# Optimization experiments

Hardware: AMD Instinct MI355X
Metric: run time of the kernel (lower is better)

## Reference

```python
import jax, jax.numpy as jnp
import numpy as np

N, E, FE = 20000, 160000, 500000
IN, HC, HEADS = 128, 64, 4
HEADC = HC // HEADS          # 16
DV = HEADC                   # 16
KHOP = 3
NUM_T = 128
OUT = 1
CST = 1e-5


def _lin(key, fan_in, fan_out):
    kw, kb = jax.random.split(key)
    s = 1.0 / np.sqrt(fan_in)
    W = jax.random.uniform(kw, (fan_in, fan_out), minval=-s, maxval=s, dtype=jnp.float32)
    b = jax.random.uniform(kb, (fan_out,), minval=-s, maxval=s, dtype=jnp.float32)
    return W, b


def setup_inputs() -> dict:
    key = jax.random.key(0)
    ks = jax.random.split(key, 16)
    x = jax.random.normal(ks[0], (N, IN), dtype=jnp.float32)
    edge_index = jax.random.randint(ks[1], (2, E), 0, N, dtype=jnp.int32)
    full_edge_index = jax.random.randint(ks[2], (2, FE), 0, N, dtype=jnp.int32)
    time_steps = jax.random.randint(ks[3], (N,), 0, NUM_T, dtype=jnp.int32)
    Wi, bi = _lin(ks[4], IN, HC)
    Wt1, bt1 = _lin(ks[5], HC, 4 * HC)
    Wt2, bt2 = _lin(ks[6], 4 * HC, HC)
    WQ, bQ = _lin(ks[7], HC, HEADS * HEADC)
    WK, bK = _lin(ks[8], HC, HEADS * HEADC)
    WV, bV = _lin(ks[9], HC, HEADS * DV)
    Wo, bo = _lin(ks[10], HEADS * DV, DV)
    hopwise = jnp.ones((KHOP + 1,), dtype=jnp.float32)
    headwise = jnp.zeros((HEADS, KHOP), dtype=jnp.float32)
    Wf1, bf1 = _lin(ks[11], 2 * DV, DV)
    Wf2, bf2 = _lin(ks[12], DV, OUT)
    return dict(x=x, edge_index=edge_index, full_edge_index=full_edge_index,
                time_steps=time_steps, Wi=Wi, bi=bi, Wt1=Wt1, bt1=bt1,
                Wt2=Wt2, bt2=bt2, WQ=WQ, bQ=bQ, WK=WK, bK=bK, WV=WV, bV=bV,
                Wo=Wo, bo=bo, hopwise=hopwise, headwise=headwise,
                Wf1=Wf1, bf1=bf1, Wf2=Wf2, bf2=bf2)


def _sin_emb(t, dim, num_steps, rescale=4000.0):
    # Sinusoidal timestep embedding rescaled by num_steps (diffusion style).
    t = t.astype(jnp.float32) * (rescale / num_steps)
    half = dim // 2
    freqs = jnp.exp(-jnp.log(10000.0) / (half - 1) * jnp.arange(half, dtype=jnp.float32))
    args = t[:, None] * freqs[None, :]
    return jnp.concatenate([jnp.sin(args), jnp.cos(args)], axis=-1)


def reference(x, edge_index, full_edge_index, time_steps,
              Wi, bi, Wt1, bt1, Wt2, bt2, WQ, bQ, WK, bK, WV, bV,
              Wo, bo, hopwise, headwise, Wf1, bf1, Wf2, bf2):
    n = x.shape[0]
    row, col = edge_index[0], edge_index[1]

    # random-walk norm: deg over destination (col), norm gathered at source (row)
    deg = jax.ops.segment_sum(jnp.ones_like(col, dtype=x.dtype), col, num_segments=n)
    deg_inv = jnp.where(deg > 0, 1.0 / deg, 0.0)
    norm = deg_inv[row]                                   # [E]

    t_emb = _sin_emb(time_steps, HC, NUM_T)               # [N, HC]
    t_emb = jax.nn.silu(t_emb @ Wt1 + bt1) @ Wt2 + bt2    # [N, HC]

    h = jax.nn.relu(x @ Wi + bi + t_emb)                  # [N, HC]

    Q = (1.0 + jax.nn.elu(h @ WQ + bQ)).reshape(n, HEADS, HEADC)
    Kf = (1.0 + jax.nn.elu(h @ WK + bK)).reshape(n, HEADS, HEADC)
    V = (h @ WV + bV).reshape(n, HEADS, DV)

    M = jnp.einsum('nhi,nhj->nhij', Kf, V)                # [N, H, hc, dv]
    hidden = V * hopwise[0]
    layerwise = jax.nn.softmax(headwise, axis=0)          # softmax over heads

    for hop in range(KHOP):
        # gather-scale-scatter message passing (random walk propagation)
        M = jax.ops.segment_sum(M[row] * norm[:, None, None, None], col, num_segments=n)
        Kf = jax.ops.segment_sum(Kf[row] * norm[:, None, None], col, num_segments=n)
        H = jnp.einsum('nhi,nhij->nhj', Q, M)             # [N, H, dv]
        C = jnp.einsum('nhi,nhi->nh', Q, Kf)[..., None] + CST
        gamma = hopwise[hop + 1] * layerwise[:, hop][:, None]   # [H, 1]
        hidden = hidden + gamma * (H / C)

    # multi_concat output projection
    hidden = hidden.reshape(n, HEADS * DV) @ Wo + bo      # [N, DV]

    src, dst = full_edge_index[0], full_edge_index[1]
    he = jnp.concatenate([hidden[src], hidden[dst]], axis=-1)  # [FE, 2*DV]
    edge_logits = jax.nn.silu(he @ Wf1 + bf1) @ Wf2 + bf2      # [FE, OUT]
    return edge_logits, hidden
```

## Files before the change

### kernel.cpp

```cpp
#include <hip/hip_runtime.h>
#include <hip/hip_bf16.h>
#include <math.h>


#define HC 64
#define HEADS 4
#define HEADC 16
#define DV 16
#define KHOP 3
#define NUM_T 128
#define MSZ 1024
#define SLOTS 64
#define CST 1e-5f

typedef float f32x2 __attribute__((ext_vector_type(2)));

__device__ __forceinline__ float bf2f(unsigned short s) { return __uint_as_float(((unsigned int)s) << 16); }
__device__ __forceinline__ unsigned short f2bf(float f) {
    unsigned int u = __float_as_uint(f);
    u = (u + 0x7fffu + ((u >> 16) & 1u)) >> 16;
    return (unsigned short)u;
}
__device__ __forceinline__ unsigned int pack4fp8(float a, float b, float c, float d) {
    int r = __builtin_amdgcn_cvt_pk_fp8_f32(a, b, 0, false);
    r = __builtin_amdgcn_cvt_pk_fp8_f32(c, d, r, true);
    return (unsigned int)r;
}

__global__ void k_fill(const int* __restrict__ row, const int* __restrict__ col,
                       int* __restrict__ cnt, int* __restrict__ csr, int E) {
    int e = blockIdx.x * 256 + threadIdx.x;
    if (e >= E) return;
    int c = col[e];
    int r = row[e];
    int k = atomicAdd(&cnt[c], 1);
    if (k < SLOTS) csr[c * SLOTS + k] = r;
}

__global__ __launch_bounds__(256) void k_misc(
    const float* __restrict__ Wt1, const float* __restrict__ bt1,
    const float* __restrict__ Wt2, const float* __restrict__ bt2,
    const float* __restrict__ hopwise, const float* __restrict__ headwise,
    const int* __restrict__ cnt,
    float* __restrict__ gamma, float* __restrict__ table,
    float* __restrict__ inv_deg, int n) {
    if (blockIdx.x >= 32) {
        int i = (blockIdx.x - 32) * 256 + threadIdx.x;
        if (i < n) {
            int d = cnt[i];
            inv_deg[i] = (d > 0) ? 1.0f / (float)min(d, SLOTS) : 0.0f;
        }
        return;
    }
    if (blockIdx.x == 0 && threadIdx.x == 0) {
        for (int k = 0; k < KHOP; k++) {
            float m = -1e30f;
            for (int h2 = 0; h2 < HEADS; h2++) m = fmaxf(m, headwise[h2 * KHOP + k]);
            float ex[HEADS]; float s = 0.f;
            for (int h2 = 0; h2 < HEADS; h2++) { ex[h2] = expf(headwise[h2 * KHOP + k] - m); s += ex[h2]; }
            for (int h2 = 0; h2 < HEADS; h2++) gamma[k * HEADS + h2] = hopwise[k + 1] * ex[h2] / s;
        }
    }
    int slot = threadIdx.x >> 6;
    int j = threadIdx.x & 63;
    int tval = blockIdx.x * 4 + slot;
    __shared__ float emb_s[4][64];
    __shared__ float z1_s[4][256];
    {
        float t = (float)tval * 31.25f;
        float e;
        if (j < 32) e = sinf(t * expf(-0.2971077539347156f * (float)j));
        else        e = cosf(t * expf(-0.2971077539347156f * (float)(j - 32)));
        emb_s[slot][j] = e;
    }
    __syncthreads();
    {
        #pragma unroll
        for (int k = 0; k < 4; k++) {
            int o = j + 64 * k;
            float acc = bt1[o];
            for (int i = 0; i < 64; i++) acc += emb_s[slot][i] * Wt1[i * 256 + o];
            z1_s[slot][o] = acc / (1.f + expf(-acc));
        }
    }
    __syncthreads();
    {
        float acc = bt2[j];
        for (int i = 0; i < 256; i++) acc += z1_s[slot][i] * Wt2[i * 64 + j];
        table[tval * 64 + j] = acc;
    }
}

__global__ __launch_bounds__(256) void k_node(
    const float* __restrict__ x, const int* __restrict__ time_steps,
    const float* __restrict__ temb, const float* __restrict__ Wi,
    const float* __restrict__ bi,
    const float* __restrict__ WQ, const float* __restrict__ bQ,
    const float* __restrict__ WK, const float* __restrict__ bK,
    const float* __restrict__ WV, const float* __restrict__ bV,
    const float* __restrict__ hopwise, const float* __restrict__ inv_deg,
    float* __restrict__ Q, unsigned short* __restrict__ Kf0,
    unsigned char* __restrict__ M0, float* __restrict__ hidden, int n) {
    __shared__ float xs[16][128];
    __shared__ float hs[16][64];
    __shared__ unsigned short ksh[16][64];
    __shared__ unsigned short vsh[16][64];
    int j = threadIdx.x & 63;
    int slot = threadIdx.x >> 6;
    int nbase = blockIdx.x * 16;
    int nvalid = min(16, n - nbase);
    const float4* xg = (const float4*)(x + (size_t)nbase * 128);
    float4* xs4 = (float4*)&xs[0][0];
    for (int idx = threadIdx.x; idx < nvalid * 32; idx += 256) xs4[idx] = xg[idx];
    __syncthreads();
    int nl = slot * 4;
    {
        float acc[4];
        #pragma unroll
        for (int k = 0; k < 4; k++) acc[k] = 0.f;
        #pragma unroll 8
        for (int i = 0; i < 128; i++) {
            float w = Wi[i * 64 + j];
            #pragma unroll
            for (int k = 0; k < 4; k++) acc[k] += xs[nl + k][i] * w;
        }
        float bj = bi[j];
        #pragma unroll
        for (int k = 0; k < 4; k++) {
            int node = nbase + nl + k;
            float te = (node < n) ? temb[time_steps[node] * 64 + j] : 0.f;
            hs[nl + k][j] = fmaxf(acc[k] + bj + te, 0.f);
        }
    }
    __syncthreads();
    float aq[4], ak[4], av[4];
    #pragma unroll
    for (int k = 0; k < 4; k++) { aq[k] = bQ[j]; ak[k] = bK[j]; av[k] = bV[j]; }
    #pragma unroll 4
    for (int i = 0; i < 64; i++) {
        float wq = WQ[i * 64 + j], wk = WK[i * 64 + j], wv = WV[i * 64 + j];
        #pragma unroll
        for (int k = 0; k < 4; k++) {
            float hv = hs[nl + k][i];
            aq[k] += hv * wq; ak[k] += hv * wk; av[k] += hv * wv;
        }
    }
    float h0 = hopwise[0];
    #pragma unroll
    for (int k = 0; k < 4; k++) {
        int node = nbase + nl + k;
        float q  = 1.f + ((aq[k] > 0.f) ? aq[k] : (expf(aq[k]) - 1.f));
        float kf = 1.f + ((ak[k] > 0.f) ? ak[k] : (expf(ak[k]) - 1.f));
        float inv = (node < n) ? inv_deg[node] : 0.f;
        unsigned short kb = f2bf(kf * inv);
        ksh[nl + k][j] = kb;
        vsh[nl + k][j] = f2bf(av[k]);
        if (node < n) {
            Q[(size_t)node * 64 + j] = q;
            Kf0[(size_t)node * 64 + j] = kb;
            hidden[(size_t)node * 64 + j] = av[k] * h0;
        }
    }
    __syncthreads();
    int t = threadIdx.x;
    #pragma unroll
    for (int it = 0; it < 4; it++) {
        int offset = it * 4096 + t * 16;
        int k = offset >> 10;
        if (k >= nvalid) break;
        int r = offset & 1023;
        int h2 = r >> 8, i2 = (r >> 4) & 15;
        float kf = bf2f(ksh[k][h2 * 16 + i2]);
        const unsigned short* vr = &vsh[k][h2 * 16];
        uint4 st;
        st.x = pack4fp8(kf * bf2f(vr[0]),  kf * bf2f(vr[1]),  kf * bf2f(vr[2]),  kf * bf2f(vr[3]));
        st.y = pack4fp8(kf * bf2f(vr[4]),  kf * bf2f(vr[5]),  kf * bf2f(vr[6]),  kf * bf2f(vr[7]));
        st.z = pack4fp8(kf * bf2f(vr[8]),  kf * bf2f(vr[9]),  kf * bf2f(vr[10]), kf * bf2f(vr[11]));
        st.w = pack4fp8(kf * bf2f(vr[12]), kf * bf2f(vr[13]), kf * bf2f(vr[14]), kf * bf2f(vr[15]));
        *(uint4*)(M0 + (size_t)nbase * MSZ + offset) = st;
    }
}

__global__ __launch_bounds__(256) void k_hop(
    const unsigned char* __restrict__ Mold, const unsigned short* __restrict__ Kfold,
    const int* __restrict__ cnt, const int* __restrict__ csr,
    const float* __restrict__ inv_deg, const float* __restrict__ Q,
    const float* __restrict__ gamma,
    unsigned char* __restrict__ Mnew, unsigned short* __restrict__ Kfnew,
    float* __restrict__ hidden, int hop, int write_out,
    const float* __restrict__ Wo, const float* __restrict__ bo,
    float* __restrict__ out16, int n) {
    int group = threadIdx.x >> 7;
    int gtid  = threadIdx.x & 127;
    int node  = blockIdx.x * 2 + group;
    int off   = gtid * 8;
    __shared__ float sm[2][MSZ];
    __shared__ float sk[2][64];
    __shared__ float sh[2][64];
    bool valid = (node < n);
    float acc[8];
    #pragma unroll
    for (int t = 0; t < 8; t++) acc[t] = 0.f;
    float kacc = 0.f;
    if (valid) {
        int deg = min(cnt[node], SLOTS);
        const int* lst = csr + (size_t)node * SLOTS;
        int d = 0;
        for (; d + 4 <= deg; d += 4) {
            int s0 = lst[d + 0], s1 = lst[d + 1], s2 = lst[d + 2], s3 = lst[d + 3];
            uint2 m0 = *(const uint2*)(Mold + (size_t)s0 * MSZ + off);
            uint2 m1 = *(const uint2*)(Mold + (size_t)s1 * MSZ + off);
            uint2 m2 = *(const uint2*)(Mold + (size_t)s2 * MSZ + off);
            uint2 m3 = *(const uint2*)(Mold + (size_t)s3 * MSZ + off);
            float kr0 = 0.f, kr1 = 0.f, kr2 = 0.f, kr3 = 0.f;
            if (gtid < 64) {
                kr0 = bf2f(Kfold[(size_t)s0 * 64 + gtid]);
                kr1 = bf2f(Kfold[(size_t)s1 * 64 + gtid]);
                kr2 = bf2f(Kfold[(size_t)s2 * 64 + gtid]);
                kr3 = bf2f(Kfold[(size_t)s3 * 64 + gtid]);
            }
            const uint2 mm[4] = {m0, m1, m2, m3};
            #pragma unroll
            for (int p = 0; p < 4; p++) {
                f32x2 q;
                q = __builtin_amdgcn_cvt_pk_f32_fp8((int)mm[p].x, false); acc[0] += q.x; acc[1] += q.y;
                q = __builtin_amdgcn_cvt_pk_f32_fp8((int)mm[p].x, true);  acc[2] += q.x; acc[3] += q.y;
                q = __builtin_amdgcn_cvt_pk_f32_fp8((int)mm[p].y, false); acc[4] += q.x; acc[5] += q.y;
                q = __builtin_amdgcn_cvt_pk_f32_fp8((int)mm[p].y, true);  acc[6] += q.x; acc[7] += q.y;
            }
            if (gtid < 64) kacc += (kr0 + kr1) + (kr2 + kr3);
        }
        for (; d < deg; d++) {
            int s = lst[d];
            uint2 mv = *(const uint2*)(Mold + (size_t)s * MSZ + off);
            f32x2 q;
            q = __builtin_amdgcn_cvt_pk_f32_fp8((int)mv.x, false); acc[0] += q.x; acc[1] += q.y;
            q = __builtin_amdgcn_cvt_pk_f32_fp8((int)mv.x, true);  acc[2] += q.x; acc[3] += q.y;
            q = __builtin_amdgcn_cvt_pk_f32_fp8((int)mv.y, false); acc[4] += q.x; acc[5] += q.y;
            q = __builtin_amdgcn_cvt_pk_f32_fp8((int)mv.y, true);  acc[6] += q.x; acc[7] += q.y;
            if (gtid < 64) kacc += bf2f(Kfold[(size_t)s * 64 + gtid]);
        }
        float4* dst = (float4*)&sm[group][off];
        dst[0] = make_float4(acc[0], acc[1], acc[2], acc[3]);
        dst[1] = make_float4(acc[4], acc[5], acc[6], acc[7]);
        if (gtid < 64) sk[group][gtid] = kacc;
        if (write_out) {
            float inv = inv_deg[node];
            uint2 st;
            st.x = pack4fp8(acc[0] * inv, acc[1] * inv, acc[2] * inv, acc[3] * inv);
            st.y = pack4fp8(acc[4] * inv, acc[5] * inv, acc[6] * inv, acc[7] * inv);
            *(uint2*)(Mnew + (size_t)node * MSZ + off) = st;
            if (gtid < 64) Kfnew[(size_t)node * 64 + gtid] = f2bf(kacc * inv);
        }
    }
    __syncthreads();
    if (valid && gtid < 64) {
        int hh = gtid >> 4, j = gtid & 15;
        const float* qn = Q + (size_t)node * 64 + hh * 16;
        float C = CST, H = 0.f;
        #pragma unroll
        for (int i = 0; i < 16; i++) {
            float qv = qn[i];
            C += qv * sk[group][hh * 16 + i];
            H += qv * sm[group][hh * 256 + i * 16 + j];
        }
        float g = gamma[hop * HEADS + hh];
        float hid = hidden[(size_t)node * 64 + gtid] + g * H / C;
        if (write_out) hidden[(size_t)node * 64 + gtid] = hid;
        else sh[group][gtid] = hid;
    }
    if (!write_out) {
        __syncthreads();
        if (valid && gtid < 16) {
            float a = bo[gtid];
            #pragma unroll 8
            for (int i = 0; i < 64; i++) a += sh[group][i] * Wo[i * 16 + gtid];
            out16[(size_t)node * 16 + gtid] = a;
        }
    }
}

__global__ __launch_bounds__(256) void k_edge(
    const int* __restrict__ src, const int* __restrict__ dst,
    const float* __restrict__ hid16,
    const float* __restrict__ Wf1, const float* __restrict__ bf1,
    const float* __restrict__ Wf2, const float* __restrict__ bf2,
    float* __restrict__ out, int fe) {
    __shared__ float w1[512];
    __shared__ float b1[16];
    __shared__ float w2[16];
    __shared__ float b2s;
    int t = threadIdx.x;
    for (int i = t; i < 512; i += 256) w1[i] = Wf1[i];
    if (t < 16) { b1[t] = bf1[t]; w2[t] = Wf2[t]; }
    if (t == 0) b2s = bf2[0];
    __syncthreads();
    int e = blockIdx.x * 256 + t;
    if (e >= fe) return;
    int s = src[e], d = dst[e];
    float he[32];
    const float4* hs4 = (const float4*)(hid16 + (size_t)s * 16);
    const float4* hd4 = (const float4*)(hid16 + (size_t)d * 16);
    #pragma unroll
    for (int q = 0; q < 4; q++) {
        float4 v = hs4[q];
        he[q * 4 + 0] = v.x; he[q * 4 + 1] = v.y; he[q * 4 + 2] = v.z; he[q * 4 + 3] = v.w;
        float4 w = hd4[q];
        he[16 + q * 4 + 0] = w.x; he[16 + q * 4 + 1] = w.y; he[16 + q * 4 + 2] = w.z; he[16 + q * 4 + 3] = w.w;
    }
    float acc = b2s;
    #pragma unroll
    for (int o = 0; o < 16; o++) {
        float z = b1[o];
        #pragma unroll
        for (int i = 0; i < 32; i++) z += he[i] * w1[i * 16 + o];
        z = z / (1.f + expf(-z));
        acc += z * w2[o];
    }
    out[e] = acc;
}

extern "C" void kernel_launch(void* const* d_in, const int* in_sizes, int n_in,
                              void* d_out, int out_size, void* d_ws, size_t ws_size,
                              hipStream_t stream) {
    const float* x        = (const float*)d_in[0];
    const int*   eidx     = (const int*)d_in[1];
    const int*   feidx    = (const int*)d_in[2];
    const int*   tsteps   = (const int*)d_in[3];
    const float* Wi  = (const float*)d_in[4];
    const float* bi  = (const float*)d_in[5];
    const float* Wt1 = (const float*)d_in[6];
    const float* bt1 = (const float*)d_in[7];
    const float* Wt2 = (const float*)d_in[8];
    const float* bt2 = (const float*)d_in[9];
    const float* WQ  = (const float*)d_in[10];
    const float* bQ  = (const float*)d_in[11];
    const float* WK  = (const float*)d_in[12];
    const float* bK  = (const float*)d_in[13];
    const float* WV  = (const float*)d_in[14];
    const float* bV  = (const float*)d_in[15];
    const float* Wo  = (const float*)d_in[16];
    const float* bo  = (const float*)d_in[17];
    const float* hopwise  = (const float*)d_in[18];
    const float* headwise = (const float*)d_in[19];
    const float* Wf1 = (const float*)d_in[20];
    const float* bf1 = (const float*)d_in[21];
    const float* Wf2 = (const float*)d_in[22];
    const float* bf2 = (const float*)d_in[23];

    const int N  = in_sizes[3];
    const int E  = in_sizes[1] / 2;
    const int FE = in_sizes[2] / 2;
    const int* row = eidx;
    const int* col = eidx + E;
    const int* fsrc = feidx;
    const int* fdst = feidx + FE;

    char* ws = (char*)d_ws;
    size_t off = 0;
    auto alloc = [&](size_t bytes) -> char* {
        char* p = ws + off;
        off = (off + bytes + 255) & ~(size_t)255;
        return p;
    };
    float* gamma     = (float*)alloc(KHOP * HEADS * sizeof(float));
    int*   cnt       = (int*)alloc((size_t)N * 4);
    int*   csr       = (int*)alloc((size_t)N * SLOTS * 4);
    float* inv_deg   = (float*)alloc((size_t)N * 4);
    float* temb      = (float*)alloc((size_t)NUM_T * HC * 4);
    float* Qbuf      = (float*)alloc((size_t)N * HC * 4);
    unsigned short* Kf0  = (unsigned short*)alloc((size_t)N * HC * 2);
    unsigned short* Kf_a = (unsigned short*)alloc((size_t)N * HC * 2);
    unsigned short* Kf_b = (unsigned short*)alloc((size_t)N * HC * 2);
    float* hidden    = (float*)alloc((size_t)N * HC * 4);
    unsigned char* M_0 = (unsigned char*)alloc((size_t)N * MSZ);
    unsigned char* M_a = (unsigned char*)alloc((size_t)N * MSZ);
    unsigned char* M_b = (unsigned char*)alloc((size_t)N * MSZ);
    (void)ws_size;

    float* out_edges = (float*)d_out;
    float* out_hid16 = (float*)d_out + FE;

    const int miscBlocks = 32 + (N + 255) / 256;
    const int hopBlocks = (N + 1) / 2;

    (void)hipMemsetAsync(cnt, 0, (size_t)N * 4, stream);
    k_fill<<<(E + 255) / 256, 256, 0, stream>>>(row, col, cnt, csr, E);
    k_misc<<<miscBlocks, 256, 0, stream>>>(Wt1, bt1, Wt2, bt2, hopwise, headwise,
                                           cnt, gamma, temb, inv_deg, N);
    k_node<<<(N + 15) / 16, 256, 0, stream>>>(x, tsteps, temb, Wi, bi,
                                              WQ, bQ, WK, bK, WV, bV, hopwise, inv_deg,
                                              Qbuf, Kf0, M_0, hidden, N);
    k_hop<<<hopBlocks, 256, 0, stream>>>(M_0, Kf0, cnt, csr, inv_deg, Qbuf, gamma,
                                         M_a, Kf_a, hidden, 0, 1, Wo, bo, out_hid16, N);
    k_hop<<<hopBlocks, 256, 0, stream>>>(M_a, Kf_a, cnt, csr, inv_deg, Qbuf, gamma,
                                         M_b, Kf_b, hidden, 1, 1, Wo, bo, out_hid16, N);
    k_hop<<<hopBlocks, 256, 0, stream>>>(M_b, Kf_b, cnt, csr, inv_deg, Qbuf, gamma,
                                         M_a, Kf_a, hidden, 2, 0, Wo, bo, out_hid16, N);
    k_edge<<<(FE + 255) / 256, 256, 0, stream>>>(fsrc, fdst, out_hid16, Wf1, bf1, Wf2, bf2,
                                                 out_edges, FE);
}
```

Before: 274.5 us.

## Skip materializing M0, wave-per-node hop gather, precompute edge MLP first layer per node

The node kernel no longer builds the 1KB-per-node fp8 outer-product M0; it stores V in bf16, and the first hop computes sum(Kf*V) directly from the neighbours' K and V rows. The hop kernel is restructured to one wave per node, with the neighbour list read once into a register and broadcast per lane, a fixed gather depth with masked tails, and shuffle-based reductions replacing shared memory and block barriers. The final hop also projects hidden through Wo and splits Wf1 into per-node src and dst partial products, so the edge kernel only adds two 16-wide vectors before SiLU. This removes a large write and read of M0 and most of the per-edge matmul work, at the cost of many shuffles and higher register pressure.

```diff
diff --git a/kernel.cpp b/kernel.cpp
--- a/kernel.cpp
+++ b/kernel.cpp
@@ -1,12 +1,9 @@
 #include <hip/hip_runtime.h>
-#include <hip/hip_bf16.h>
 #include <math.h>
 
 
 #define HC 64
 #define HEADS 4
-#define HEADC 16
-#define DV 16
 #define KHOP 3
 #define NUM_T 128
 #define MSZ 1024
@@ -16,6 +13,8 @@
 typedef float f32x2 __attribute__((ext_vector_type(2)));
 
 __device__ __forceinline__ float bf2f(unsigned short s) { return __uint_as_float(((unsigned int)s) << 16); }
+__device__ __forceinline__ float bfu_lo(unsigned int u) { return __uint_as_float(u << 16); }
+__device__ __forceinline__ float bfu_hi(unsigned int u) { return __uint_as_float(u & 0xffff0000u); }
 __device__ __forceinline__ unsigned short f2bf(float f) {
     unsigned int u = __float_as_uint(f);
     u = (u + 0x7fffu + ((u >> 16) & 1u)) >> 16;
@@ -100,11 +99,9 @@
     const float* __restrict__ WV, const float* __restrict__ bV,
     const float* __restrict__ hopwise, const float* __restrict__ inv_deg,
     float* __restrict__ Q, unsigned short* __restrict__ Kf0,
-    unsigned char* __restrict__ M0, float* __restrict__ hidden, int n) {
+    unsigned short* __restrict__ Vbuf, float* __restrict__ hidden, int n) {
     __shared__ float xs[16][128];
     __shared__ float hs[16][64];
-    __shared__ unsigned short ksh[16][64];
-    __shared__ unsigned short vsh[16][64];
     int j = threadIdx.x & 63;
     int slot = threadIdx.x >> 6;
     int nbase = blockIdx.x * 16;
@@ -149,173 +146,213 @@
     #pragma unroll
     for (int k = 0; k < 4; k++) {
         int node = nbase + nl + k;
-        float q  = 1.f + ((aq[k] > 0.f) ? aq[k] : (expf(aq[k]) - 1.f));
-        float kf = 1.f + ((ak[k] > 0.f) ? ak[k] : (expf(ak[k]) - 1.f));
-        float inv = (node < n) ? inv_deg[node] : 0.f;
-        unsigned short kb = f2bf(kf * inv);
-        ksh[nl + k][j] = kb;
-        vsh[nl + k][j] = f2bf(av[k]);
         if (node < n) {
+            float q  = 1.f + ((aq[k] > 0.f) ? aq[k] : (expf(aq[k]) - 1.f));
+            float kf = 1.f + ((ak[k] > 0.f) ? ak[k] : (expf(ak[k]) - 1.f));
+            float inv = inv_deg[node];
             Q[(size_t)node * 64 + j] = q;
-            Kf0[(size_t)node * 64 + j] = kb;
+            Kf0[(size_t)node * 64 + j] = f2bf(kf * inv);
+            Vbuf[(size_t)node * 64 + j] = f2bf(av[k]);
             hidden[(size_t)node * 64 + j] = av[k] * h0;
         }
     }
-    __syncthreads();
-    int t = threadIdx.x;
-    #pragma unroll
-    for (int it = 0; it < 4; it++) {
-        int offset = it * 4096 + t * 16;
-        int k = offset >> 10;
-        if (k >= nvalid) break;
-        int r = offset & 1023;
-        int h2 = r >> 8, i2 = (r >> 4) & 15;
-        float kf = bf2f(ksh[k][h2 * 16 + i2]);
-        const unsigned short* vr = &vsh[k][h2 * 16];
-        uint4 st;
-        st.x = pack4fp8(kf * bf2f(vr[0]),  kf * bf2f(vr[1]),  kf * bf2f(vr[2]),  kf * bf2f(vr[3]));
-        st.y = pack4fp8(kf * bf2f(vr[4]),  kf * bf2f(vr[5]),  kf * bf2f(vr[6]),  kf * bf2f(vr[7]));
-        st.z = pack4fp8(kf * bf2f(vr[8]),  kf * bf2f(vr[9]),  kf * bf2f(vr[10]), kf * bf2f(vr[11]));
-        st.w = pack4fp8(kf * bf2f(vr[12]), kf * bf2f(vr[13]), kf * bf2f(vr[14]), kf * bf2f(vr[15]));
-        *(uint4*)(M0 + (size_t)nbase * MSZ + offset) = st;
-    }
-}
-
+}
+
+template<int MODE>
 __global__ __launch_bounds__(256) void k_hop(
     const unsigned char* __restrict__ Mold, const unsigned short* __restrict__ Kfold,
+    const unsigned short* __restrict__ Vbuf,
     const int* __restrict__ cnt, const int* __restrict__ csr,
     const float* __restrict__ inv_deg, const float* __restrict__ Q,
     const float* __restrict__ gamma,
     unsigned char* __restrict__ Mnew, unsigned short* __restrict__ Kfnew,
     float* __restrict__ hidden, int hop, int write_out,
     const float* __restrict__ Wo, const float* __restrict__ bo,
-    float* __restrict__ out16, int n) {
-    int group = threadIdx.x >> 7;
-    int gtid  = threadIdx.x & 127;
-    int node  = blockIdx.x * 2 + group;
-    int off   = gtid * 8;
-    __shared__ float sm[2][MSZ];
-    __shared__ float sk[2][64];
-    __shared__ float sh[2][64];
-    bool valid = (node < n);
-    float acc[8];
-    #pragma unroll
-    for (int t = 0; t < 8; t++) acc[t] = 0.f;
+    const float* __restrict__ Wf1, float* __restrict__ out16,
+    float* __restrict__ Pbuf, int n) {
+    constexpr int DEPTH = (MODE == 0) ? 4 : 8;
+    int lane = threadIdx.x & 63;
+    int node = blockIdx.x * 4 + (threadIdx.x >> 6);
+    if (node >= n) return;
+    int grp = lane >> 4;
+    int deg = min(cnt[node], SLOTS);
+    int degU = __builtin_amdgcn_readfirstlane(deg);
+    int sidx = csr[(size_t)node * SLOTS + lane];
+    float qv = Q[(size_t)node * 64 + lane];
+    float acc[16];
+    #pragma unroll
+    for (int t = 0; t < 16; t++) acc[t] = 0.f;
     float kacc = 0.f;
-    if (valid) {
-        int deg = min(cnt[node], SLOTS);
-        const int* lst = csr + (size_t)node * SLOTS;
-        int d = 0;
-        for (; d + 4 <= deg; d += 4) {
-            int s0 = lst[d + 0], s1 = lst[d + 1], s2 = lst[d + 2], s3 = lst[d + 3];
-            uint2 m0 = *(const uint2*)(Mold + (size_t)s0 * MSZ + off);
-            uint2 m1 = *(const uint2*)(Mold + (size_t)s1 * MSZ + off);
-            uint2 m2 = *(const uint2*)(Mold + (size_t)s2 * MSZ + off);
-            uint2 m3 = *(const uint2*)(Mold + (size_t)s3 * MSZ + off);
-            float kr0 = 0.f, kr1 = 0.f, kr2 = 0.f, kr3 = 0.f;
-            if (gtid < 64) {
-                kr0 = bf2f(Kfold[(size_t)s0 * 64 + gtid]);
-                kr1 = bf2f(Kfold[(size_t)s1 * 64 + gtid]);
-                kr2 = bf2f(Kfold[(size_t)s2 * 64 + gtid]);
-                kr3 = bf2f(Kfold[(size_t)s3 * 64 + gtid]);
+
+    for (int base = 0; base < degU; base += DEPTH) {
+        unsigned short kraw[DEPTH];
+        uint4 m0[DEPTH], m1[DEPTH];
+        #pragma unroll
+        for (int t = 0; t < DEPTH; t++) {
+            int d = base + t;
+            int dc = (d < degU) ? d : (degU - 1);
+            int s = __builtin_amdgcn_readlane(sidx, dc);
+            kraw[t] = Kfold[(size_t)s * 64 + lane];
+            if constexpr (MODE == 0) {
+                const uint4* vp = (const uint4*)((const unsigned char*)Vbuf + (size_t)s * 128 + grp * 32);
+                m0[t] = vp[0];
+                m1[t] = vp[1];
+            } else {
+                m0[t] = *(const uint4*)(Mold + (size_t)s * MSZ + lane * 16);
             }
-            const uint2 mm[4] = {m0, m1, m2, m3};
+        }
+        #pragma unroll
+        for (int t = 0; t < DEPTH; t++) {
+            float wt = (base + t < degU) ? 1.f : 0.f;
+            float kf = bf2f(kraw[t]);
+            kacc = fmaf(wt, kf, kacc);
+            if constexpr (MODE == 0) {
+                float kw = kf * wt;
+                acc[0]  = fmaf(kw, bfu_lo(m0[t].x), acc[0]);
+                acc[1]  = fmaf(kw, bfu_hi(m0[t].x), acc[1]);
+                acc[2]  = fmaf(kw, bfu_lo(m0[t].y), acc[2]);
+                acc[3]  = fmaf(kw, bfu_hi(m0[t].y), acc[3]);
+                acc[4]  = fmaf(kw, bfu_lo(m0[t].z), acc[4]);
+                acc[5]  = fmaf(kw, bfu_hi(m0[t].z), acc[5]);
+                acc[6]  = fmaf(kw, bfu_lo(m0[t].w), acc[6]);
+                acc[7]  = fmaf(kw, bfu_hi(m0[t].w), acc[7]);
+                acc[8]  = fmaf(kw, bfu_lo(m1[t].x), acc[8]);
+                acc[9]  = fmaf(kw, bfu_hi(m1[t].x), acc[9]);
+                acc[10] = fmaf(kw, bfu_lo(m1[t].y), acc[10]);
+                acc[11] = fmaf(kw, bfu_hi(m1[t].y), acc[11]);
+                acc[12] = fmaf(kw, bfu_lo(m1[t].z), acc[12]);
+                acc[13] = fmaf(kw, bfu_hi(m1[t].z), acc[13]);
+                acc[14] = fmaf(kw, bfu_lo(m1[t].w), acc[14]);
+                acc[15] = fmaf(kw, bfu_hi(m1[t].w), acc[15]);
+            } else {
+                f32x2 p;
+                p = __builtin_amdgcn_cvt_pk_f32_fp8((int)m0[t].x, false); acc[0]  = fmaf(wt, p.x, acc[0]);  acc[1]  = fmaf(wt, p.y, acc[1]);
+                p = __builtin_amdgcn_cvt_pk_f32_fp8((int)m0[t].x, true);  acc[2]  = fmaf(wt, p.x, acc[2]);  acc[3]  = fmaf(wt, p.y, acc[3]);
+                p = __builtin_amdgcn_cvt_pk_f32_fp8((int)m0[t].y, false); acc[4]  = fmaf(wt, p.x, acc[4]);  acc[5]  = fmaf(wt, p.y, acc[5]);
+                p = __builtin_amdgcn_cvt_pk_f32_fp8((int)m0[t].y, true);  acc[6]  = fmaf(wt, p.x, acc[6]);  acc[7]  = fmaf(wt, p.y, acc[7]);
+                p = __builtin_amdgcn_cvt_pk_f32_fp8((int)m0[t].z, false); acc[8]  = fmaf(wt, p.x, acc[8]);  acc[9]  = fmaf(wt, p.y, acc[9]);
+                p = __builtin_amdgcn_cvt_pk_f32_fp8((int)m0[t].z, true);  acc[10] = fmaf(wt, p.x, acc[10]); acc[11] = fmaf(wt, p.y, acc[11]);
+                p = __builtin_amdgcn_cvt_pk_f32_fp8((int)m0[t].w, false); acc[12] = fmaf(wt, p.x, acc[12]); acc[13] = fmaf(wt, p.y, acc[13]);
+                p = __builtin_amdgcn_cvt_pk_f32_fp8((int)m0[t].w, true);  acc[14] = fmaf(wt, p.x, acc[14]); acc[15] = fmaf(wt, p.y, acc[15]);
+            }
+        }
+    }
+
+    if (write_out) {
+        float inv = inv_deg[node];
+        uint4 st;
+        st.x = pack4fp8(acc[0] * inv,  acc[1] * inv,  acc[2] * inv,  acc[3] * inv);
+        st.y = pack4fp8(acc[4] * inv,  acc[5] * inv,  acc[6] * inv,  acc[7] * inv);
+        st.z = pack4fp8(acc[8] * inv,  acc[9] * inv,  acc[10] * inv, acc[11] * inv);
+        st.w = pack4fp8(acc[12] * inv, acc[13] * inv, acc[14] * inv, acc[15] * inv);
+        *(uint4*)(Mnew + (size_t)node * MSZ + lane * 16) = st;
+        Kfnew[(size_t)node * 64 + lane] = f2bf(kacc * inv);
+    }
+
+    float c = qv * kacc;
+    c += __shfl_xor(c, 1); c += __shfl_xor(c, 2); c += __shfl_xor(c, 4); c += __shfl_xor(c, 8);
+
+    float w0[16];
+    #pragma unroll
+    for (int t = 0; t < 16; t++) w0[t] = qv * acc[t];
+    float w1r[8];
+    #pragma unroll
+    for (int t = 0; t < 8; t++) {
+        float a = w0[2 * t], b = w0[2 * t + 1];
+        float mine = (lane & 1) ? b : a, th = (lane & 1) ? a : b;
+        w1r[t] = mine + __shfl_xor(th, 1);
+    }
+    float w2r[4];
+    #pragma unroll
+    for (int t = 0; t < 4; t++) {
+        float a = w1r[2 * t], b = w1r[2 * t + 1];
+        float mine = (lane & 2) ? b : a, th = (lane & 2) ? a : b;
+        w2r[t] = mine + __shfl_xor(th, 2);
+    }
+    float w3r[2];
+    #pragma unroll
+    for (int t = 0; t < 2; t++) {
+        float a = w2r[2 * t], b = w2r[2 * t + 1];
+        float mine = (lane & 4) ? b : a, th = (lane & 4) ? a : b;
+        w3r[t] = mine + __shfl_xor(th, 4);
+    }
+    float Hv;
+    {
+        float a = w3r[0], b = w3r[1];
+        float mine = (lane & 8) ? b : a, th = (lane & 8) ? a : b;
+        Hv = mine + __shfl_xor(th, 8);
+    }
+
+    float g = gamma[hop * HEADS + grp];
+    float contrib = g * Hv / (c + CST);
+    size_t hoff = (size_t)node * 64 + lane;
+    if (write_out) {
+        hidden[hoff] = hidden[hoff] + contrib;
+    } else {
+        float hid = hidden[hoff] + contrib;
+        const float4* wop = (const float4*)(Wo + lane * 16);
+        float4 wo0 = wop[0], wo1 = wop[1], wo2 = wop[2], wo3 = wop[3];
+        float v[16];
+        v[0] = hid * wo0.x;  v[1] = hid * wo0.y;  v[2] = hid * wo0.z;  v[3] = hid * wo0.w;
+        v[4] = hid * wo1.x;  v[5] = hid * wo1.y;  v[6] = hid * wo1.z;  v[7] = hid * wo1.w;
+        v[8] = hid * wo2.x;  v[9] = hid * wo2.y;  v[10] = hid * wo2.z; v[11] = hid * wo2.w;
+        v[12] = hid * wo3.x; v[13] = hid * wo3.y; v[14] = hid * wo3.z; v[15] = hid * wo3.w;
+        #pragma unroll
+        for (int m = 32; m >= 1; m >>= 1) {
             #pragma unroll
-            for (int p = 0; p < 4; p++) {
-                f32x2 q;
-                q = __builtin_amdgcn_cvt_pk_f32_fp8((int)mm[p].x, false); acc[0] += q.x; acc[1] += q.y;
-                q = __builtin_amdgcn_cvt_pk_f32_fp8((int)mm[p].x, true);  acc[2] += q.x; acc[3] += q.y;
-                q = __builtin_amdgcn_cvt_pk_f32_fp8((int)mm[p].y, false); acc[4] += q.x; acc[5] += q.y;
-                q = __builtin_amdgcn_cvt_pk_f32_fp8((int)mm[p].y, true);  acc[6] += q.x; acc[7] += q.y;
-            }
-            if (gtid < 64) kacc += (kr0 + kr1) + (kr2 + kr3);
-        }
-        for (; d < deg; d++) {
-            int s = lst[d];
-            uint2 mv = *(const uint2*)(Mold + (size_t)s * MSZ + off);
-            f32x2 q;
-            q = __builtin_amdgcn_cvt_pk_f32_fp8((int)mv.x, false); acc[0] += q.x; acc[1] += q.y;
-            q = __builtin_amdgcn_cvt_pk_f32_fp8((int)mv.x, true);  acc[2] += q.x; acc[3] += q.y;
-            q = __builtin_amdgcn_cvt_pk_f32_fp8((int)mv.y, false); acc[4] += q.x; acc[5] += q.y;
-            q = __builtin_amdgcn_cvt_pk_f32_fp8((int)mv.y, true);  acc[6] += q.x; acc[7] += q.y;
-            if (gtid < 64) kacc += bf2f(Kfold[(size_t)s * 64 + gtid]);
-        }
-        float4* dst = (float4*)&sm[group][off];
-        dst[0] = make_float4(acc[0], acc[1], acc[2], acc[3]);
-        dst[1] = make_float4(acc[4], acc[5], acc[6], acc[7]);
-        if (gtid < 64) sk[group][gtid] = kacc;
-        if (write_out) {
-            float inv = inv_deg[node];
-            uint2 st;
-            st.x = pack4fp8(acc[0] * inv, acc[1] * inv, acc[2] * inv, acc[3] * inv);
-            st.y = pack4fp8(acc[4] * inv, acc[5] * inv, acc[6] * inv, acc[7] * inv);
-            *(uint2*)(Mnew + (size_t)node * MSZ + off) = st;
-            if (gtid < 64) Kfnew[(size_t)node * 64 + gtid] = f2bf(kacc * inv);
-        }
-    }
-    __syncthreads();
-    if (valid && gtid < 64) {
-        int hh = gtid >> 4, j = gtid & 15;
-        const float* qn = Q + (size_t)node * 64 + hh * 16;
-        float C = CST, H = 0.f;
-        #pragma unroll
-        for (int i = 0; i < 16; i++) {
-            float qv = qn[i];
-            C += qv * sk[group][hh * 16 + i];
-            H += qv * sm[group][hh * 256 + i * 16 + j];
-        }
-        float g = gamma[hop * HEADS + hh];
-        float hid = hidden[(size_t)node * 64 + gtid] + g * H / C;
-        if (write_out) hidden[(size_t)node * 64 + gtid] = hid;
-        else sh[group][gtid] = hid;
-    }
-    if (!write_out) {
-        __syncthreads();
-        if (valid && gtid < 16) {
-            float a = bo[gtid];
-            #pragma unroll 8
-            for (int i = 0; i < 64; i++) a += sh[group][i] * Wo[i * 16 + gtid];
-            out16[(size_t)node * 16 + gtid] = a;
+            for (int o = 0; o < 16; o++) v[o] += __shfl_xor(v[o], m);
+        }
+        #pragma unroll
+        for (int o = 0; o < 16; o++) v[o] += bo[o];
+        if (lane == 0) {
+            float4* op = (float4*)(out16 + (size_t)node * 16);
+            op[0] = make_float4(v[0],  v[1],  v[2],  v[3]);
+            op[1] = make_float4(v[4],  v[5],  v[6],  v[7]);
+            op[2] = make_float4(v[8],  v[9],  v[10], v[11]);
+            op[3] = make_float4(v[12], v[13], v[14], v[15]);
+        }
+        if (lane < 32) {
+            int o = lane & 15, half = lane >> 4;
+            const float* wf = Wf1 + (size_t)(half * 16) * 16 + o;
+            float p = 0.f;
+            #pragma unroll
+            for (int i = 0; i < 16; i++) p += v[i] * wf[i * 16];
+            Pbuf[(size_t)node * 32 + lane] = p;
         }
     }
 }
 
 __global__ __launch_bounds__(256) void k_edge(
     const int* __restrict__ src, const int* __restrict__ dst,
-    const float* __restrict__ hid16,
-    const float* __restrict__ Wf1, const float* __restrict__ bf1,
-    const float* __restrict__ Wf2, const float* __restrict__ bf2,
+    const float* __restrict__ Pbuf,
+    const float* __restrict__ bf1, const float* __restrict__ Wf2,
+    const float* __restrict__ bf2,
     float* __restrict__ out, int fe) {
-    __shared__ float w1[512];
     __shared__ float b1[16];
     __shared__ float w2[16];
     __shared__ float b2s;
     int t = threadIdx.x;
-    for (int i = t; i < 512; i += 256) w1[i] = Wf1[i];
     if (t < 16) { b1[t] = bf1[t]; w2[t] = Wf2[t]; }
     if (t == 0) b2s = bf2[0];
     __syncthreads();
     int e = blockIdx.x * 256 + t;
     if (e >= fe) return;
     int s = src[e], d = dst[e];
-    float he[32];
-    const float4* hs4 = (const float4*)(hid16 + (size_t)s * 16);
-    const float4* hd4 = (const float4*)(hid16 + (size_t)d * 16);
+    const float4* p1 = (const float4*)(Pbuf + (size_t)s * 32);
+    const float4* p2 = (const float4*)(Pbuf + (size_t)d * 32 + 16);
+    float z[16];
     #pragma unroll
     for (int q = 0; q < 4; q++) {
-        float4 v = hs4[q];
-        he[q * 4 + 0] = v.x; he[q * 4 + 1] = v.y; he[q * 4 + 2] = v.z; he[q * 4 + 3] = v.w;
-        float4 w = hd4[q];
-        he[16 + q * 4 + 0] = w.x; he[16 + q * 4 + 1] = w.y; he[16 + q * 4 + 2] = w.z; he[16 + q * 4 + 3] = w.w;
+        float4 a = p1[q]; float4 b = p2[q];
+        z[q * 4 + 0] = a.x + b.x; z[q * 4 + 1] = a.y + b.y;
+        z[q * 4 + 2] = a.z + b.z; z[q * 4 + 3] = a.w + b.w;
     }
     float acc = b2s;
     #pragma unroll
     for (int o = 0; o < 16; o++) {
-        float z = b1[o];
-        #pragma unroll
-        for (int i = 0; i < 32; i++) z += he[i] * w1[i * 16 + o];
-        z = z / (1.f + expf(-z));
-        acc += z * w2[o];
+        float zz = z[o] + b1[o];
+        zz = zz / (1.f + expf(-zz));
+        acc += zz * w2[o];
     }
     out[e] = acc;
 }
@@ -372,17 +409,18 @@
     unsigned short* Kf0  = (unsigned short*)alloc((size_t)N * HC * 2);
     unsigned short* Kf_a = (unsigned short*)alloc((size_t)N * HC * 2);
     unsigned short* Kf_b = (unsigned short*)alloc((size_t)N * HC * 2);
+    unsigned short* Vbuf = (unsigned short*)alloc((size_t)N * HC * 2);
     float* hidden    = (float*)alloc((size_t)N * HC * 4);
-    unsigned char* M_0 = (unsigned char*)alloc((size_t)N * MSZ);
     unsigned char* M_a = (unsigned char*)alloc((size_t)N * MSZ);
     unsigned char* M_b = (unsigned char*)alloc((size_t)N * MSZ);
+    float* Pbuf      = (float*)alloc((size_t)N * 32 * 4);
     (void)ws_size;
 
     float* out_edges = (float*)d_out;
     float* out_hid16 = (float*)d_out + FE;
 
     const int miscBlocks = 32 + (N + 255) / 256;
-    const int hopBlocks = (N + 1) / 2;
+    const int hopBlocks = (N + 3) / 4;
 
     (void)hipMemsetAsync(cnt, 0, (size_t)N * 4, stream);
     k_fill<<<(E + 255) / 256, 256, 0, stream>>>(row, col, cnt, csr, E);
@@ -390,13 +428,13 @@
                                            cnt, gamma, temb, inv_deg, N);
     k_node<<<(N + 15) / 16, 256, 0, stream>>>(x, tsteps, temb, Wi, bi,
                                               WQ, bQ, WK, bK, WV, bV, hopwise, inv_deg,
-                                              Qbuf, Kf0, M_0, hidden, N);
-    k_hop<<<hopBlocks, 256, 0, stream>>>(M_0, Kf0, cnt, csr, inv_deg, Qbuf, gamma,
-                                         M_a, Kf_a, hidden, 0, 1, Wo, bo, out_hid16, N);
-    k_hop<<<hopBlocks, 256, 0, stream>>>(M_a, Kf_a, cnt, csr, inv_deg, Qbuf, gamma,
-                                         M_b, Kf_b, hidden, 1, 1, Wo, bo, out_hid16, N);
-    k_hop<<<hopBlocks, 256, 0, stream>>>(M_b, Kf_b, cnt, csr, inv_deg, Qbuf, gamma,
-                                         M_a, Kf_a, hidden, 2, 0, Wo, bo, out_hid16, N);
-    k_edge<<<(FE + 255) / 256, 256, 0, stream>>>(fsrc, fdst, out_hid16, Wf1, bf1, Wf2, bf2,
+                                              Qbuf, Kf0, Vbuf, hidden, N);
+    k_hop<0><<<hopBlocks, 256, 0, stream>>>(nullptr, Kf0, Vbuf, cnt, csr, inv_deg, Qbuf, gamma,
+                                            M_a, Kf_a, hidden, 0, 1, Wo, bo, Wf1, out_hid16, Pbuf, N);
+    k_hop<1><<<hopBlocks, 256, 0, stream>>>(M_a, Kf_a, nullptr, cnt, csr, inv_deg, Qbuf, gamma,
+                                            M_b, Kf_b, hidden, 1, 1, Wo, bo, Wf1, out_hid16, Pbuf, N);
+    k_hop<1><<<hopBlocks, 256, 0, stream>>>(M_b, Kf_b, nullptr, cnt, csr, inv_deg, Qbuf, gamma,
+                                            M_a, Kf_a, hidden, 2, 0, Wo, bo, Wf1, out_hid16, Pbuf, N);
+    k_edge<<<(FE + 255) / 256, 256, 0, stream>>>(fsrc, fdst, Pbuf, bf1, Wf2, bf2,
                                                  out_edges, FE);
 }
```

New measurement: 270.3 us. About the same (-1.5%).
